# Kernel optimization log

Hardware: AMD Instinct MI355X
Metric: run time of the kernel (lower is better)

The kernel has to match this reference:

```python
import jax, jax.numpy as jnp
import numpy as np

EPS = 1e-12  # torch F.normalize eps

def _cam(fmap, w):
    # torch: sum over C of w[1,C,R,1,1] * fmap[B,C,1,H,W] -> (B,R,H,W)
    # expressed as an efficient contraction (1x1 conv / GEMM)
    return jnp.einsum('bchw,rc->brhw', fmap, w)

def _embedding(fmap, w, b):
    pooled = fmap.mean(axis=(-2, -1))           # (B,C) AdaptiveAvgPool2d(1)
    return pooled @ w.T + b                      # (B,R)

def _certainty(cam):
    B, R = cam.shape[:2]
    flat = cam.reshape(B, R, -1)
    return jnp.std(flat, axis=-1, ddof=1)        # torch .std() is unbiased

def _avgpool_to(x, out_hw):
    # adaptive avg pool with integer ratio == reshape-mean
    B, R, H, W = x.shape
    oh, ow = out_hw
    return x.reshape(B, R, oh, H // oh, ow, W // ow).mean(axis=(3, 5))

def _link(low_cam, high_cam):
    low_cam = jax.lax.stop_gradient(low_cam)
    high_cam = jax.lax.stop_gradient(high_cam)
    if low_cam.shape[2:] != high_cam.shape[2:]:
        low_cam = _avgpool_to(low_cam, high_cam.shape[2:])
    B = low_cam.shape[0]
    lo = low_cam.reshape(B, low_cam.shape[1], -1)
    hi = high_cam.reshape(B, high_cam.shape[1], -1)
    lo = lo / jnp.maximum(jnp.linalg.norm(lo, axis=-1, keepdims=True), EPS)
    hi = hi / jnp.maximum(jnp.linalg.norm(hi, axis=-1, keepdims=True), EPS)
    return jnp.einsum('bmi,bni->mn', lo, hi) / B

def setup_inputs() -> dict:
    key = jax.random.key(0)
    ks = jax.random.split(key, 6)
    B, R = 64, 128
    chans = [512, 1024, 2048]
    hws = [28, 14, 7]
    inp = {}
    for l in range(3):
        inp[f'fmap{l}'] = jax.random.normal(ks[l], (B, chans[l], hws[l], hws[l]), dtype=jnp.float32)
        inp[f'w{l}'] = jax.random.normal(ks[3 + l], (R, chans[l]), dtype=jnp.float32) * 0.02
        inp[f'b{l}'] = jnp.zeros((R,), dtype=jnp.float32)
    return inp

def reference(fmap0, fmap1, fmap2, w0, b0, w1, b1, w2, b2):
    fmaps = [fmap0, fmap1, fmap2]
    ws = [w0, w1, w2]
    bs = [b0, b1, b2]
    embeddings = [_embedding(f, w, b) for f, w, b in zip(fmaps, ws, bs)]
    cams = [_cam(f, w) for f, w in zip(fmaps, ws)]
    certainties = [_certainty(c) for c in cams]
    links = [_link(cams[l - 1], cams[l]) for l in range(1, 3)]
    return (*embeddings, *certainties, *links)
```

## Files before the change

kernel.cpp:

```cpp
#include <hip/hip_runtime.h>
#include <stdint.h>

#define R 128
#define NB 64

#define CAM0_OFF 0
#define CAM1_OFF 6422528
#define CAM2_OFF 8028160
#define POOL0_OFF 8429568
#define POOL1_OFF 10035200
#define WB_OFF    10436608
#define PART_OFF  10665984

typedef __bf16 bf16;
typedef bf16 v8bf __attribute__((ext_vector_type(8)));
typedef float f4v __attribute__((ext_vector_type(4)));

__global__ void prep_w(const float* __restrict__ w0, const float* __restrict__ w1,
                       const float* __restrict__ w2, bf16* __restrict__ wb) {
    int id = blockIdx.x * 256 + threadIdx.x;
    float v;
    if (id < 65536)       v = w0[id];
    else if (id < 196608) v = w1[id - 65536];
    else                  v = w2[id - 196608];
    wb[id] = (bf16)v;
}

__global__ __launch_bounds__(256) void cam_gemm(
    const float* __restrict__ f0, const float* __restrict__ f1,
    const float* __restrict__ f2, const bf16* __restrict__ wb,
    float* __restrict__ ws) {
    __shared__ bf16  ldsA[128 * 72];
    __shared__ float ldsB[64 * 64];

    int bid = blockIdx.x, tid = threadIdx.x;
    int lvl, tile;
    if (bid < 49)       { lvl = 2; tile = bid; }
    else if (bid < 245) { lvl = 1; tile = bid - 49; }
    else                { lvl = 0; tile = bid - 245; }
    const int C  = (lvl == 0) ? 512 : (lvl == 1) ? 1024 : 2048;
    const int HW = (lvl == 0) ? 784 : (lvl == 1) ? 196  : 49;
    const float* fmap = (lvl == 0) ? f0 : (lvl == 1) ? f1 : f2;
    const bf16*  wbl  = wb + ((lvl == 0) ? 0 : (lvl == 1) ? 65536 : 196608);
    float* cam = ws + ((lvl == 0) ? CAM0_OFF : (lvl == 1) ? CAM1_OFF : CAM2_OFF);
    const int n0 = tile * 64;

    int boff[4][4];
    int bldsoff[4];
#pragma unroll
    for (int pass = 0; pass < 4; ++pass) {
        int ch = pass * 256 + tid;
        int k = ch >> 4, c = ch & 15;
        int p = (c + ((k >> 3) & 3) * 4) & 15;
        bldsoff[pass] = k * 64 + p * 4;
#pragma unroll
        for (int e = 0; e < 4; ++e) {
            int n = n0 + c * 4 + e;
            int b = n / HW, i = n - b * HW;
            boff[pass][e] = b * C * HW + i + k * HW;
        }
    }
    const int lane = tid & 63, wave = tid >> 6;
    const int lm = lane & 15, q = lane >> 4;
    const int wm = (wave >> 1) * 64, wn = (wave & 1) * 32;
    int bIdx[2], bv[2], iv[2];
#pragma unroll
    for (int sn = 0; sn < 2; ++sn) {
        int nl = wn + sn * 16 + lm;
        int P = ((nl >> 2) + 4 * q) & 15;
        bIdx[sn] = P * 4 + (nl & 3);
        int n = n0 + nl;
        bv[sn] = n / HW; iv[sn] = n - bv[sn] * HW;
    }

    f4v acc[4][2] = {};
    for (int kc = 0; kc < C; kc += 64) {
#pragma unroll
        for (int pass = 0; pass < 4; ++pass) {
            int ch = pass * 256 + tid;
            int r = ch >> 3, ko = (ch & 7) * 8;
            *(int4*)&ldsA[r * 72 + ko] = *(const int4*)&wbl[r * C + kc + ko];
        }
        int kb = kc * HW;
#pragma unroll
        for (int pass = 0; pass < 4; ++pass) {
            float4 v;
            v.x = fmap[boff[pass][0] + kb];
            v.y = fmap[boff[pass][1] + kb];
            v.z = fmap[boff[pass][2] + kb];
            v.w = fmap[boff[pass][3] + kb];
            *(float4*)&ldsB[bldsoff[pass]] = v;
        }
        __syncthreads();
#pragma unroll
        for (int ks = 0; ks < 64; ks += 32) {
            v8bf af[4];
#pragma unroll
            for (int sm = 0; sm < 4; ++sm)
                af[sm] = *(const v8bf*)&ldsA[(wm + sm * 16 + lm) * 72 + ks + q * 8];
            v8bf bfr[2];
#pragma unroll
            for (int sn = 0; sn < 2; ++sn) {
#pragma unroll
                for (int j = 0; j < 8; ++j)
                    bfr[sn][j] = (bf16)ldsB[(ks + q * 8 + j) * 64 + bIdx[sn]];
            }
#pragma unroll
            for (int sm = 0; sm < 4; ++sm)
#pragma unroll
                for (int sn = 0; sn < 2; ++sn)
                    acc[sm][sn] = __builtin_amdgcn_mfma_f32_16x16x32_bf16(
                        af[sm], bfr[sn], acc[sm][sn], 0, 0, 0);
        }
        __syncthreads();
    }
#pragma unroll
    for (int sn = 0; sn < 2; ++sn) {
        int base = (bv[sn] * R) * HW + iv[sn];
#pragma unroll
        for (int sm = 0; sm < 4; ++sm) {
#pragma unroll
            for (int reg = 0; reg < 4; ++reg) {
                int r = wm + sm * 16 + q * 4 + reg;
                cam[base + r * HW] = acc[sm][sn][reg];
            }
        }
    }
}

__global__ __launch_bounds__(256) void stats_k(
    const float* __restrict__ ws, const float* __restrict__ b0,
    const float* __restrict__ b1, const float* __restrict__ b2,
    float* __restrict__ out) {
    int gw = blockIdx.x * 4 + (threadIdx.x >> 6);
    int lane = threadIdx.x & 63;
    int lvl = gw >> 13, row = gw & 8191;
    const int HW = (lvl == 0) ? 784 : (lvl == 1) ? 196 : 49;
    const float* cam = ws + ((lvl == 0) ? CAM0_OFF : (lvl == 1) ? CAM1_OFF : CAM2_OFF)
                        + (long)row * HW;
    float s = 0.f, ss = 0.f;
    for (int j = lane; j < HW; j += 64) { float v = cam[j]; s += v; ss += v * v; }
#pragma unroll
    for (int o = 32; o; o >>= 1) { s += __shfl_xor(s, o); ss += __shfl_xor(ss, o); }
    if (lane == 0) {
        const float* bias = (lvl == 0) ? b0 : (lvl == 1) ? b1 : b2;
        float mean = s / (float)HW;
        out[lvl * 8192 + row] = mean + bias[row & 127];
        float var = fmaxf(ss - s * mean, 0.f) / (float)(HW - 1);
        out[24576 + lvl * 8192 + row] = sqrtf(var);
    }
}

__global__ void pool_k(float* __restrict__ ws) {
    int id = blockIdx.x * 256 + threadIdx.x;
    if (id < 1605632) {
        int ow = id % 14, t1 = id / 14; int oh = t1 % 14; int row = t1 / 14;
        const float* src = ws + CAM0_OFF + (long)row * 784;
        int i0 = oh * 56 + ow * 2;
        ws[POOL0_OFF + id] = (src[i0] + src[i0 + 1] + src[i0 + 28] + src[i0 + 29]) * 0.25f;
    } else {
        int id2 = id - 1605632;
        int ow = id2 % 7, t1 = id2 / 7; int oh = t1 % 7; int row = t1 / 7;
        const float* src = ws + CAM1_OFF + (long)row * 196;
        int i0 = oh * 28 + ow * 2;
        ws[POOL1_OFF + id2] = (src[i0] + src[i0 + 1] + src[i0 + 14] + src[i0 + 15]) * 0.25f;
    }
}

__global__ __launch_bounds__(256) void normscale_k(float* __restrict__ ws) {
    int gw = blockIdx.x * 4 + (threadIdx.x >> 6);
    int lane = threadIdx.x & 63;
    int op = gw >> 13, row = gw & 8191;
    float* p; int K;
    if (op == 0)      { p = ws + POOL0_OFF + (long)row * 196; K = 196; }
    else if (op == 1) { p = ws + CAM1_OFF + (long)row * 196; K = 196; }
    else if (op == 2) { p = ws + POOL1_OFF + (long)row * 49; K = 49; }
    else              { p = ws + CAM2_OFF + (long)row * 49; K = 49; }
    float ss = 0.f;
    for (int j = lane; j < K; j += 64) { float v = p[j]; ss += v * v; }
#pragma unroll
    for (int o = 32; o; o >>= 1) ss += __shfl_xor(ss, o);
    float inv = 1.0f / fmaxf(sqrtf(ss), 1e-12f);
    for (int j = lane; j < K; j += 64) p[j] *= inv;
}

__global__ __launch_bounds__(256) void link_k(const float* __restrict__ ws,
                                              float* __restrict__ part) {
    extern __shared__ float lds[];
    float* hiT = lds;
    float* loT = lds + 196 * 68;
    int bid = blockIdx.x, tid = threadIdx.x;
    int lk = bid >> 9, rem = bid & 511;
    int b = rem >> 3, mq = (rem >> 1) & 3, nh = rem & 1;
    const int K = lk ? 49 : 196;
    const float* lo = ws + (lk ? POOL1_OFF : POOL0_OFF) + (long)(b * 128 + mq * 32) * K;
    const float* hi = ws + (lk ? CAM2_OFF : CAM1_OFF) + (long)(b * 128 + nh * 64) * K;
    for (int idx = tid; idx < 64 * K; idx += 256) {
        int nr = idx / K, i = idx - nr * K;
        hiT[i * 68 + nr] = hi[idx];
    }
    for (int idx = tid; idx < 32 * K; idx += 256) {
        int mr = idx / K, i = idx - mr * K;
        loT[i * 36 + mr] = lo[idx];
    }
    __syncthreads();
    int tm = tid >> 5, tn = tid & 31;
    int m0 = tm * 4, n0 = tn * 2;
    float a0x = 0, a0y = 0, a1x = 0, a1y = 0, a2x = 0, a2y = 0, a3x = 0, a3y = 0;
    for (int i = 0; i < K; ++i) {
        float4 lv = *(const float4*)&loT[i * 36 + m0];
        float2 hv = *(const float2*)&hiT[i * 68 + n0];
        a0x += lv.x * hv.x; a0y += lv.x * hv.y;
        a1x += lv.y * hv.x; a1y += lv.y * hv.y;
        a2x += lv.z * hv.x; a2y += lv.z * hv.y;
        a3x += lv.w * hv.x; a3y += lv.w * hv.y;
    }
    float* dst = part + lk * 1048576 + b * 16384 + (mq * 32 + m0) * 128 + nh * 64 + n0;
    dst[0] = a0x; dst[1] = a0y;
    dst[128] = a1x; dst[129] = a1y;
    dst[256] = a2x; dst[257] = a2y;
    dst[384] = a3x; dst[385] = a3y;
}

__global__ void linkred_k(const float* __restrict__ part, float* __restrict__ out) {
    int id = blockIdx.x * 256 + threadIdx.x;
    int lk = id >> 14, mn = id & 16383;
    const float* p = part + lk * 1048576 + mn;
    float s = 0.f;
#pragma unroll 8
    for (int b = 0; b < 64; ++b) s += p[b * 16384];
    out[49152 + lk * 16384 + mn] = s * (1.0f / 64.0f);
}

extern "C" void kernel_launch(void* const* d_in, const int* in_sizes, int n_in,
                              void* d_out, int out_size, void* d_ws, size_t ws_size,
                              hipStream_t stream) {
    const float* f0 = (const float*)d_in[0];
    const float* w0 = (const float*)d_in[1];
    const float* b0 = (const float*)d_in[2];
    const float* f1 = (const float*)d_in[3];
    const float* w1 = (const float*)d_in[4];
    const float* b1 = (const float*)d_in[5];
    const float* f2 = (const float*)d_in[6];
    const float* w2 = (const float*)d_in[7];
    const float* b2 = (const float*)d_in[8];
    float* ws = (float*)d_ws;
    float* out = (float*)d_out;
    bf16* wb = (bf16*)(ws + WB_OFF);

    prep_w<<<1792, 256, 0, stream>>>(w0, w1, w2, wb);
    cam_gemm<<<1029, 256, 0, stream>>>(f0, f1, f2, wb, ws);
    stats_k<<<6144, 256, 0, stream>>>(ws, b0, b1, b2, out);
    pool_k<<<7840, 256, 0, stream>>>(ws);
    normscale_k<<<8192, 256, 0, stream>>>(ws);
    link_k<<<1024, 256, 81536, stream>>>(ws, ws + PART_OFF);
    linkred_k<<<128, 256, 0, stream>>>(ws + PART_OFF, out);
}
```

Measured before the change: 312.2 us.

## Drop LDS staging in CAM GEMM, fuse pooling with normalization, chunk link LDS

The CAM GEMM now loads weight fragments and feature-map columns directly from global memory into MFMA operands, with no LDS tiles and no barriers. Average pooling is fused with L2 normalization into one kernel, so the remaining normscale pass only handles the high-level cams. The link kernel processes K in chunks of 49 with small static LDS buffers, which lowers the per-block shared memory footprint. This trades LDS reuse in the GEMM for cache reliance and uncoalesced-ish strided loads, which may raise global traffic.

New measurement: 356.3 us. 14.1% more time.

```diff
diff --git a/kernel.cpp b/kernel.cpp
--- a/kernel.cpp
+++ b/kernel.cpp
@@ -30,9 +30,6 @@
     const float* __restrict__ f0, const float* __restrict__ f1,
     const float* __restrict__ f2, const bf16* __restrict__ wb,
     float* __restrict__ ws) {
-    __shared__ bf16  ldsA[128 * 72];
-    __shared__ float ldsB[64 * 64];
-
     int bid = blockIdx.x, tid = threadIdx.x;
     int lvl, tile;
     if (bid < 49)       { lvl = 2; tile = bid; }
@@ -45,74 +42,43 @@
     float* cam = ws + ((lvl == 0) ? CAM0_OFF : (lvl == 1) ? CAM1_OFF : CAM2_OFF);
     const int n0 = tile * 64;
 
-    int boff[4][4];
-    int bldsoff[4];
-#pragma unroll
-    for (int pass = 0; pass < 4; ++pass) {
-        int ch = pass * 256 + tid;
-        int k = ch >> 4, c = ch & 15;
-        int p = (c + ((k >> 3) & 3) * 4) & 15;
-        bldsoff[pass] = k * 64 + p * 4;
-#pragma unroll
-        for (int e = 0; e < 4; ++e) {
-            int n = n0 + c * 4 + e;
-            int b = n / HW, i = n - b * HW;
-            boff[pass][e] = b * C * HW + i + k * HW;
-        }
-    }
     const int lane = tid & 63, wave = tid >> 6;
     const int lm = lane & 15, q = lane >> 4;
     const int wm = (wave >> 1) * 64, wn = (wave & 1) * 32;
-    int bIdx[2], bv[2], iv[2];
+
+    int bv[2], iv[2], bbase[2];
 #pragma unroll
     for (int sn = 0; sn < 2; ++sn) {
-        int nl = wn + sn * 16 + lm;
-        int P = ((nl >> 2) + 4 * q) & 15;
-        bIdx[sn] = P * 4 + (nl & 3);
-        int n = n0 + nl;
+        int n = n0 + wn + sn * 16 + lm;
         bv[sn] = n / HW; iv[sn] = n - bv[sn] * HW;
-    }
+        bbase[sn] = bv[sn] * C * HW + iv[sn] + q * 8 * HW;
+    }
+    const bf16* arow[4];
+#pragma unroll
+    for (int sm = 0; sm < 4; ++sm)
+        arow[sm] = wbl + (wm + sm * 16 + lm) * C + q * 8;
 
     f4v acc[4][2] = {};
-    for (int kc = 0; kc < C; kc += 64) {
-#pragma unroll
-        for (int pass = 0; pass < 4; ++pass) {
-            int ch = pass * 256 + tid;
-            int r = ch >> 3, ko = (ch & 7) * 8;
-            *(int4*)&ldsA[r * 72 + ko] = *(const int4*)&wbl[r * C + kc + ko];
-        }
-        int kb = kc * HW;
-#pragma unroll
-        for (int pass = 0; pass < 4; ++pass) {
-            float4 v;
-            v.x = fmap[boff[pass][0] + kb];
-            v.y = fmap[boff[pass][1] + kb];
-            v.z = fmap[boff[pass][2] + kb];
-            v.w = fmap[boff[pass][3] + kb];
-            *(float4*)&ldsB[bldsoff[pass]] = v;
-        }
-        __syncthreads();
-#pragma unroll
-        for (int ks = 0; ks < 64; ks += 32) {
-            v8bf af[4];
-#pragma unroll
-            for (int sm = 0; sm < 4; ++sm)
-                af[sm] = *(const v8bf*)&ldsA[(wm + sm * 16 + lm) * 72 + ks + q * 8];
-            v8bf bfr[2];
-#pragma unroll
-            for (int sn = 0; sn < 2; ++sn) {
-#pragma unroll
-                for (int j = 0; j < 8; ++j)
-                    bfr[sn][j] = (bf16)ldsB[(ks + q * 8 + j) * 64 + bIdx[sn]];
-            }
-#pragma unroll
-            for (int sm = 0; sm < 4; ++sm)
-#pragma unroll
-                for (int sn = 0; sn < 2; ++sn)
-                    acc[sm][sn] = __builtin_amdgcn_mfma_f32_16x16x32_bf16(
-                        af[sm], bfr[sn], acc[sm][sn], 0, 0, 0);
-        }
-        __syncthreads();
+#pragma unroll 2
+    for (int kc = 0; kc < C; kc += 32) {
+        v8bf af[4];
+#pragma unroll
+        for (int sm = 0; sm < 4; ++sm)
+            af[sm] = *(const v8bf*)(arow[sm] + kc);
+        v8bf bfr[2];
+#pragma unroll
+        for (int sn = 0; sn < 2; ++sn) {
+            int base = bbase[sn] + kc * HW;
+#pragma unroll
+            for (int j = 0; j < 8; ++j)
+                bfr[sn][j] = (bf16)fmap[base + j * HW];
+        }
+#pragma unroll
+        for (int sm = 0; sm < 4; ++sm)
+#pragma unroll
+            for (int sn = 0; sn < 2; ++sn)
+                acc[sm][sn] = __builtin_amdgcn_mfma_f32_16x16x32_bf16(
+                    af[sm], bfr[sn], acc[sm][sn], 0, 0, 0);
     }
 #pragma unroll
     for (int sn = 0; sn < 2; ++sn) {
@@ -151,20 +117,29 @@
     }
 }
 
-__global__ void pool_k(float* __restrict__ ws) {
-    int id = blockIdx.x * 256 + threadIdx.x;
-    if (id < 1605632) {
-        int ow = id % 14, t1 = id / 14; int oh = t1 % 14; int row = t1 / 14;
-        const float* src = ws + CAM0_OFF + (long)row * 784;
-        int i0 = oh * 56 + ow * 2;
-        ws[POOL0_OFF + id] = (src[i0] + src[i0 + 1] + src[i0 + 28] + src[i0 + 29]) * 0.25f;
-    } else {
-        int id2 = id - 1605632;
-        int ow = id2 % 7, t1 = id2 / 7; int oh = t1 % 7; int row = t1 / 7;
-        const float* src = ws + CAM1_OFF + (long)row * 196;
-        int i0 = oh * 28 + ow * 2;
-        ws[POOL1_OFF + id2] = (src[i0] + src[i0 + 1] + src[i0 + 14] + src[i0 + 15]) * 0.25f;
-    }
+__global__ __launch_bounds__(256) void pool_norm_k(float* __restrict__ ws) {
+    int gw = blockIdx.x * 4 + (threadIdx.x >> 6);
+    int lane = threadIdx.x & 63;
+    int op = gw >> 13, row = gw & 8191;
+    const float* src = ws + (op == 0 ? CAM0_OFF : CAM1_OFF)
+                        + (long)row * (op == 0 ? 784 : 196);
+    float* dst = ws + (op == 0 ? POOL0_OFF : POOL1_OFF)
+                    + (long)row * (op == 0 ? 196 : 49);
+    const int OP = op == 0 ? 196 : 49;
+    const int OW = op == 0 ? 14 : 7;
+    const int IW = op == 0 ? 28 : 14;
+    float vals[4]; float ss = 0.f; int cnt = 0;
+    for (int p = lane; p < OP; p += 64) {
+        int oh = p / OW, ow = p - oh * OW;
+        int i0 = oh * 2 * IW + ow * 2;
+        float v = (src[i0] + src[i0 + 1] + src[i0 + IW] + src[i0 + IW + 1]) * 0.25f;
+        vals[cnt++] = v; ss += v * v;
+    }
+#pragma unroll
+    for (int o = 32; o; o >>= 1) ss += __shfl_xor(ss, o);
+    float inv = 1.0f / fmaxf(sqrtf(ss), 1e-12f);
+    cnt = 0;
+    for (int p = lane; p < OP; p += 64) dst[p] = vals[cnt++] * inv;
 }
 
 __global__ __launch_bounds__(256) void normscale_k(float* __restrict__ ws) {
@@ -172,10 +147,8 @@
     int lane = threadIdx.x & 63;
     int op = gw >> 13, row = gw & 8191;
     float* p; int K;
-    if (op == 0)      { p = ws + POOL0_OFF + (long)row * 196; K = 196; }
-    else if (op == 1) { p = ws + CAM1_OFF + (long)row * 196; K = 196; }
-    else if (op == 2) { p = ws + POOL1_OFF + (long)row * 49; K = 49; }
-    else              { p = ws + CAM2_OFF + (long)row * 49; K = 49; }
+    if (op == 0) { p = ws + CAM1_OFF + (long)row * 196; K = 196; }
+    else         { p = ws + CAM2_OFF + (long)row * 49;  K = 49; }
     float ss = 0.f;
     for (int j = lane; j < K; j += 64) { float v = p[j]; ss += v * v; }
 #pragma unroll
@@ -186,34 +159,37 @@
 
 __global__ __launch_bounds__(256) void link_k(const float* __restrict__ ws,
                                               float* __restrict__ part) {
-    extern __shared__ float lds[];
-    float* hiT = lds;
-    float* loT = lds + 196 * 68;
+    __shared__ float hiT[49 * 68];
+    __shared__ float loT[49 * 36];
     int bid = blockIdx.x, tid = threadIdx.x;
     int lk = bid >> 9, rem = bid & 511;
     int b = rem >> 3, mq = (rem >> 1) & 3, nh = rem & 1;
     const int K = lk ? 49 : 196;
     const float* lo = ws + (lk ? POOL1_OFF : POOL0_OFF) + (long)(b * 128 + mq * 32) * K;
     const float* hi = ws + (lk ? CAM2_OFF : CAM1_OFF) + (long)(b * 128 + nh * 64) * K;
-    for (int idx = tid; idx < 64 * K; idx += 256) {
-        int nr = idx / K, i = idx - nr * K;
-        hiT[i * 68 + nr] = hi[idx];
-    }
-    for (int idx = tid; idx < 32 * K; idx += 256) {
-        int mr = idx / K, i = idx - mr * K;
-        loT[i * 36 + mr] = lo[idx];
-    }
-    __syncthreads();
     int tm = tid >> 5, tn = tid & 31;
     int m0 = tm * 4, n0 = tn * 2;
     float a0x = 0, a0y = 0, a1x = 0, a1y = 0, a2x = 0, a2y = 0, a3x = 0, a3y = 0;
-    for (int i = 0; i < K; ++i) {
-        float4 lv = *(const float4*)&loT[i * 36 + m0];
-        float2 hv = *(const float2*)&hiT[i * 68 + n0];
-        a0x += lv.x * hv.x; a0y += lv.x * hv.y;
-        a1x += lv.y * hv.x; a1y += lv.y * hv.y;
-        a2x += lv.z * hv.x; a2y += lv.z * hv.y;
-        a3x += lv.w * hv.x; a3y += lv.w * hv.y;
+    for (int ic = 0; ic < K; ic += 49) {
+        for (int idx = tid; idx < 64 * 49; idx += 256) {
+            int nr = idx / 49, i = idx - nr * 49;
+            hiT[i * 68 + nr] = hi[nr * K + ic + i];
+        }
+        for (int idx = tid; idx < 32 * 49; idx += 256) {
+            int mr = idx / 49, i = idx - mr * 49;
+            loT[i * 36 + mr] = lo[mr * K + ic + i];
+        }
+        __syncthreads();
+#pragma unroll 7
+        for (int i = 0; i < 49; ++i) {
+            float4 lv = *(const float4*)&loT[i * 36 + m0];
+            float2 hv = *(const float2*)&hiT[i * 68 + n0];
+            a0x += lv.x * hv.x; a0y += lv.x * hv.y;
+            a1x += lv.y * hv.x; a1y += lv.y * hv.y;
+            a2x += lv.z * hv.x; a2y += lv.z * hv.y;
+            a3x += lv.w * hv.x; a3y += lv.w * hv.y;
+        }
+        __syncthreads();
     }
     float* dst = part + lk * 1048576 + b * 16384 + (mq * 32 + m0) * 128 + nh * 64 + n0;
     dst[0] = a0x; dst[1] = a0y;
@@ -251,8 +227,8 @@
     prep_w<<<1792, 256, 0, stream>>>(w0, w1, w2, wb);
     cam_gemm<<<1029, 256, 0, stream>>>(f0, f1, f2, wb, ws);
     stats_k<<<6144, 256, 0, stream>>>(ws, b0, b1, b2, out);
-    pool_k<<<7840, 256, 0, stream>>>(ws);
-    normscale_k<<<8192, 256, 0, stream>>>(ws);
-    link_k<<<1024, 256, 81536, stream>>>(ws, ws + PART_OFF);
+    pool_norm_k<<<4096, 256, 0, stream>>>(ws);
+    normscale_k<<<4096, 256, 0, stream>>>(ws);
+    link_k<<<1024, 256, 0, stream>>>(ws, ws + PART_OFF);
     linkred_k<<<128, 256, 0, stream>>>(ws + PART_OFF, out);
 }
```
